# Kernel optimization log

Measured on AMD Instinct MI355X. Metric: run time of the kernel, lower is better.

Reference implementation:

```python
import jax, jax.numpy as jnp
import numpy as np

N = 50000      # nodes
E = 1_600_000  # edges
F_IN = 128; HID = 128; LAT = 64; OUT = 128; GEN = 2


def gcn_conv(x, src, dst, norm, W, b, n_nodes):
    """PyG GCNConv with self-loops already appended to (src, dst) and
    symmetric normalization `norm` precomputed per edge."""
    h = x @ W                                    # [N, out]
    msg = h[src] * norm[:, None]                 # [E+N, out] gather + scale
    out = jax.ops.segment_sum(msg, dst, num_segments=n_nodes)
    return out + b


def _self_loop_norm(edge_index, n_nodes):
    loops = jnp.arange(n_nodes, dtype=edge_index.dtype)
    src = jnp.concatenate([edge_index[0], loops])
    dst = jnp.concatenate([edge_index[1], loops])
    deg = jnp.zeros((n_nodes,), jnp.float32).at[dst].add(1.0)
    dinv = jnp.where(deg > 0, deg ** -0.5, 0.0)
    norm = dinv[src] * dinv[dst]
    return src, dst, norm


def setup_inputs() -> dict:
    key = jax.random.key(0)
    ks = jax.random.split(key, 12)
    p = lambda k, s: jax.random.normal(k, s, jnp.float32) * 0.05
    return {
        "x": jax.random.normal(ks[0], (N, F_IN), jnp.float32),
        "edge_index": jax.random.randint(ks[1], (2, E), 0, N, jnp.int32),
        "eps": jax.random.normal(ks[2], (N, LAT), jnp.float32),
        "u": jax.random.uniform(ks[3], (N, GEN), jnp.float32),
        "W1": p(ks[4], (F_IN, HID)), "b1": jnp.zeros((HID,), jnp.float32),
        "W_mu": p(ks[5], (HID, LAT)), "b_mu": jnp.zeros((LAT,), jnp.float32),
        "W_ls": p(ks[6], (HID, LAT)), "b_ls": jnp.zeros((LAT,), jnp.float32),
        "W_dx": p(ks[7], (LAT, OUT)), "b_dx": jnp.zeros((OUT,), jnp.float32),
        "W_g": p(ks[8], (LAT, GEN)), "b_g": jnp.zeros((GEN,), jnp.float32),
        "W_lc": p(ks[9], (LAT, 1)), "b_lc": jnp.zeros((1,), jnp.float32),
    }


def reference(x, edge_index, eps, u, W1, b1, W_mu, b_mu, W_ls, b_ls,
              W_dx, b_dx, W_g, b_g, W_lc, b_lc):
    n = x.shape[0]
    src, dst, norm = _self_loop_norm(edge_index, n)

    # Encoder: GCN -> relu -> (mu, logvar)
    h = jax.nn.relu(gcn_conv(x, src, dst, norm, W1, b1, n))
    mu = gcn_conv(h, src, dst, norm, W_mu, b_mu, n)
    logvar = gcn_conv(h, src, dst, norm, W_ls, b_ls, n)

    # reparameterize: z = eps * exp(0.5*logvar) + mu
    z = eps * jnp.exp(0.5 * logvar) + mu

    # decoders / classifiers
    recon_x = gcn_conv(z, src, dst, norm, W_dx, b_dx, n)
    logits_gender = gcn_conv(z, src, dst, norm, W_g, b_g, n)
    logits_label = z @ W_lc + b_lc

    # Gumbel-softmax (hard, straight-through), temperature=1.0
    g = -jnp.log(-jnp.log(u + 1e-20) + 1e-20)
    y_soft = jax.nn.softmax(logits_gender + g, axis=-1)
    y_hard = jax.nn.one_hot(jnp.argmax(y_soft, axis=-1), GEN, dtype=y_soft.dtype)
    gender = jax.lax.stop_gradient(y_hard - y_soft) + y_soft

    return (recon_x, gender, logits_label, mu, logvar, z)
```

## Files before the change

### kernel.cpp

```cpp
#include <hip/hip_runtime.h>
#include <hip/hip_fp16.h>
#include <cstddef>


constexpr int R = 200;
constexpr int NBUCK = 250;
constexpr int NBLK = 250;
constexpr int SLABCAP = 12288;

__global__ __launch_bounds__(256, 4) void hist_gemm_kernel(
    const int* __restrict__ dst, int* __restrict__ gh, int e, int chunk,
    const float* __restrict__ A, const float* __restrict__ W,
    __half* __restrict__ Ch, int n) {
  constexpr int K = 128, M = 128, KT = 64, RPT = 4;
  constexpr int CG = M / 4;
  constexpr int RS = 256 / CG;
  constexpr int RPB = RS * RPT;
  __shared__ float sW[KT * M];
  __shared__ int h[NBUCK];

  if (blockIdx.x < (unsigned)NBLK) {
    for (int t = threadIdx.x; t < NBUCK; t += 256) h[t] = 0;
    __syncthreads();
    int beg = blockIdx.x * chunk;
    int fin = min(e, beg + chunk);
    for (int i = beg + threadIdx.x; i < fin; i += 256)
      atomicAdd(&h[dst[i] / R], 1);
    __syncthreads();
    for (int t = threadIdx.x; t < NBUCK; t += 256)
      gh[t * NBLK + blockIdx.x] = h[t];
    return;
  }

  const int bid = blockIdx.x - NBLK;
  const int cg = threadIdx.x % CG;
  const int rs = threadIdx.x / CG;
  const int row0 = bid * RPB + rs * RPT;

  const float* Arow[RPT];
#pragma unroll
  for (int rr = 0; rr < RPT; ++rr) {
    int row = row0 + rr;
    if (row > n - 1) row = n - 1;
    Arow[rr] = A + (size_t)row * K;
  }

  float4 acc[RPT];
#pragma unroll
  for (int rr = 0; rr < RPT; ++rr) acc[rr] = float4{0.f, 0.f, 0.f, 0.f};

  for (int kt = 0; kt < K; kt += KT) {
    if (kt) __syncthreads();
    for (int i = threadIdx.x * 4; i < KT * M; i += 1024)
      *reinterpret_cast<float4*>(&sW[i]) =
          *reinterpret_cast<const float4*>(&W[kt * M + i]);
    __syncthreads();
#pragma unroll 4
    for (int k4 = 0; k4 < KT; k4 += 4) {
      float4 a[RPT];
#pragma unroll
      for (int rr = 0; rr < RPT; ++rr)
        a[rr] = *reinterpret_cast<const float4*>(Arow[rr] + kt + k4);
#pragma unroll
      for (int j = 0; j < 4; ++j) {
        float4 w = *reinterpret_cast<const float4*>(&sW[(k4 + j) * M + cg * 4]);
#pragma unroll
        for (int rr = 0; rr < RPT; ++rr) {
          float av = reinterpret_cast<const float*>(&a[rr])[j];
          acc[rr].x += av * w.x;
          acc[rr].y += av * w.y;
          acc[rr].z += av * w.z;
          acc[rr].w += av * w.w;
        }
      }
    }
  }

#pragma unroll
  for (int rr = 0; rr < RPT; ++rr) {
    int row = row0 + rr;
    if (row < n) {
      __half2* d2 = reinterpret_cast<__half2*>(Ch + (size_t)row * M + cg * 4);
      d2[0] = __floats2half2_rn(acc[rr].x, acc[rr].y);
      d2[1] = __floats2half2_rn(acc[rr].z, acc[rr].w);
    }
  }
}

__global__ __launch_bounds__(256) void bscan_kernel(
    const int* __restrict__ gh, int* __restrict__ ghs,
    int* __restrict__ rowptr_n) {
  __shared__ int s[256];
  __shared__ int sBase[NBUCK + 1];
  const int b = blockIdx.x;
  const int tid = threadIdx.x;

  int tot = 0;
  if (tid < NBUCK) {
    const int* row = gh + tid * NBLK;
    for (int k = 0; k < NBLK; ++k) tot += row[k];
  }
  s[tid] = tot;
  __syncthreads();
  for (int off = 1; off < 256; off <<= 1) {
    int t = (tid >= off) ? s[tid - off] : 0;
    __syncthreads();
    s[tid] += t;
    __syncthreads();
  }
  if (tid < NBUCK) sBase[tid] = s[tid] - tot;
  if (tid == NBUCK - 1) sBase[NBUCK] = s[tid];
  __syncthreads();

  int v = (tid < NBLK) ? gh[b * NBLK + tid] : 0;
  s[tid] = v;
  __syncthreads();
  for (int off = 1; off < 256; off <<= 1) {
    int t = (tid >= off) ? s[tid - off] : 0;
    __syncthreads();
    s[tid] += t;
    __syncthreads();
  }
  if (tid < NBLK) ghs[b * NBLK + tid] = s[tid] - v + sBase[b];
  if (b == 0 && tid == 0) *rowptr_n = sBase[NBUCK];
}

__global__ __launch_bounds__(256) void scatter_kernel(
    const int* __restrict__ src, const int* __restrict__ dst,
    const int* __restrict__ ghs, int* __restrict__ binned, int e, int chunk) {
  __shared__ int cur[NBUCK];
  for (int t = threadIdx.x; t < NBUCK; t += 256)
    cur[t] = ghs[t * NBLK + blockIdx.x];
  __syncthreads();
  int beg = blockIdx.x * chunk;
  int fin = min(e, beg + chunk);
  for (int i = beg + threadIdx.x; i < fin; i += 256) {
    int d = dst[i];
    int b = d / R;
    int p = atomicAdd(&cur[b], 1);
    binned[p] = ((d - b * R) << 16) | src[i];
  }
}

__global__ __launch_bounds__(256) void final_kernel(
    const int* __restrict__ binned, const int* __restrict__ ghs,
    int* __restrict__ rowptr, int* __restrict__ csr,
    float* __restrict__ dinv, int n, int e) {
  __shared__ int sdeg[R];
  __shared__ int sscan[256];
  __shared__ int scur[R];
  __shared__ int slab[SLABCAP];
  const int b = blockIdx.x;
  const int tid = threadIdx.x;
  const int base = ghs[b * NBLK];
  const int end = (b < NBUCK - 1) ? ghs[(b + 1) * NBLK] : e;
  const int cnt = end - base;

  if (tid < R) sdeg[tid] = 0;
  __syncthreads();
  for (int k = base + tid; k < end; k += 256)
    atomicAdd(&sdeg[binned[k] >> 16], 1);
  __syncthreads();

  int dv = (tid < R) ? sdeg[tid] : 0;
  sscan[tid] = dv;
  __syncthreads();
  for (int off = 1; off < 256; off <<= 1) {
    int t = (tid >= off) ? sscan[tid - off] : 0;
    __syncthreads();
    sscan[tid] += t;
    __syncthreads();
  }
  int excl = sscan[tid] - dv;
  int node = b * R + tid;
  if (tid < R && node < n) {
    rowptr[node] = base + excl;
    dinv[node] = 1.0f / sqrtf((float)dv + 1.0f);
    scur[tid] = excl;
  }
  __syncthreads();

  const bool fits = (cnt <= SLABCAP);
  for (int k = base + tid; k < end; k += 256) {
    int rec = binned[k];
    int p = atomicAdd(&scur[rec >> 16], 1);
    int s = rec & 0xFFFF;
    if (fits) slab[p] = s;
    else csr[base + p] = s;
  }
  __syncthreads();
  if (fits)
    for (int k = tid; k < cnt; k += 256) csr[base + k] = slab[k];
}

template <int K, int M, int KT, int RPT, bool BIAS>
__global__ __launch_bounds__(256, 4) void gemm_kernel(
    const float* __restrict__ A, const float* __restrict__ W,
    const float* __restrict__ bias, float* __restrict__ C, int n) {
  constexpr int CG = M / 4;
  constexpr int RS = 256 / CG;
  constexpr int RPB = RS * RPT;
  __shared__ float sW[KT * M];
  const int cg = threadIdx.x % CG;
  const int rs = threadIdx.x / CG;
  const int row0 = blockIdx.x * RPB + rs * RPT;

  const float* Arow[RPT];
#pragma unroll
  for (int rr = 0; rr < RPT; ++rr) {
    int row = row0 + rr;
    if (row > n - 1) row = n - 1;
    Arow[rr] = A + (size_t)row * K;
  }

  float4 acc[RPT];
#pragma unroll
  for (int rr = 0; rr < RPT; ++rr) acc[rr] = float4{0.f, 0.f, 0.f, 0.f};

  for (int kt = 0; kt < K; kt += KT) {
    if (kt) __syncthreads();
    for (int i = threadIdx.x * 4; i < KT * M; i += 1024)
      *reinterpret_cast<float4*>(&sW[i]) =
          *reinterpret_cast<const float4*>(&W[kt * M + i]);
    __syncthreads();
#pragma unroll 4
    for (int k4 = 0; k4 < KT; k4 += 4) {
      float4 a[RPT];
#pragma unroll
      for (int rr = 0; rr < RPT; ++rr)
        a[rr] = *reinterpret_cast<const float4*>(Arow[rr] + kt + k4);
#pragma unroll
      for (int j = 0; j < 4; ++j) {
        float4 w = *reinterpret_cast<const float4*>(&sW[(k4 + j) * M + cg * 4]);
#pragma unroll
        for (int rr = 0; rr < RPT; ++rr) {
          float av = reinterpret_cast<const float*>(&a[rr])[j];
          acc[rr].x += av * w.x;
          acc[rr].y += av * w.y;
          acc[rr].z += av * w.z;
          acc[rr].w += av * w.w;
        }
      }
    }
  }

  float4 bv = float4{0.f, 0.f, 0.f, 0.f};
  if (BIAS) bv = *reinterpret_cast<const float4*>(&bias[cg * 4]);
#pragma unroll
  for (int rr = 0; rr < RPT; ++rr) {
    int row = row0 + rr;
    if (row < n) {
      float4 o = acc[rr];
      if (BIAS) { o.x += bv.x; o.y += bv.y; o.z += bv.z; o.w += bv.w; }
      *reinterpret_cast<float4*>(&C[(size_t)row * M + cg * 4]) = o;
    }
  }
}

template <bool SRCSCALE, bool BIAS, bool RELU, bool HALF_OUT>
__global__ __launch_bounds__(256) void spmm128_kernel(
    const __half* __restrict__ Xs, void* __restrict__ Yout,
    const int* __restrict__ rowptr, const int* __restrict__ csr,
    const float* __restrict__ dinv, const float* __restrict__ bias, int n) {
  int wid = (blockIdx.x * blockDim.x + threadIdx.x) >> 6;
  int lane = threadIdx.x & 63;
  if (wid >= n) return;
  int beg = rowptr[wid];
  int end = rowptr[wid + 1];
  constexpr int U = 8;
  float a0[U], a1[U];
#pragma unroll
  for (int uu = 0; uu < U; ++uu) { a0[uu] = 0.f; a1[uu] = 0.f; }

  for (int base = beg; base < end; base += 64) {
    int m = end - base;
    if (m > 64) m = 64;
    int idx = (lane < m) ? csr[base + lane] : 0;
    int j = 0;
    for (; j + U <= m; j += U) {
      const __half2* rows[U];
      float ds[U];
#pragma unroll
      for (int uu = 0; uu < U; ++uu) {
        int i = __shfl(idx, j + uu, 64);
        rows[uu] = reinterpret_cast<const __half2*>(Xs + (size_t)i * 128);
        if (SRCSCALE) ds[uu] = dinv[i];
      }
      __half2 v[U];
#pragma unroll
      for (int uu = 0; uu < U; ++uu) v[uu] = rows[uu][lane];
#pragma unroll
      for (int uu = 0; uu < U; ++uu) {
        float2 f = __half22float2(v[uu]);
        if (SRCSCALE) {
          a0[uu] += ds[uu] * f.x;
          a1[uu] += ds[uu] * f.y;
        } else {
          a0[uu] += f.x;
          a1[uu] += f.y;
        }
      }
    }
    for (; j < m; ++j) {
      int i = __shfl(idx, j, 64);
      const __half2* row = reinterpret_cast<const __half2*>(Xs + (size_t)i * 128);
      float2 f = __half22float2(row[lane]);
      if (SRCSCALE) {
        float ds = dinv[i];
        a0[0] += ds * f.x;
        a1[0] += ds * f.y;
      } else {
        a0[0] += f.x;
        a1[0] += f.y;
      }
    }
  }

  float t0 = 0.f, t1 = 0.f;
#pragma unroll
  for (int uu = 0; uu < U; ++uu) { t0 += a0[uu]; t1 += a1[uu]; }

  float di = dinv[wid];

  float2 sf = __half22float2(
      reinterpret_cast<const __half2*>(Xs + (size_t)wid * 128)[lane]);
  if (SRCSCALE) {
    t0 += di * sf.x;
    t1 += di * sf.y;
  } else {
    t0 += sf.x;
    t1 += sf.y;
  }

  float r0 = di * t0;
  float r1 = di * t1;
  if (BIAS) { r0 += bias[lane * 2]; r1 += bias[lane * 2 + 1]; }
  if (RELU) { r0 = fmaxf(r0, 0.f); r1 = fmaxf(r1, 0.f); }

  if (HALF_OUT) {
    reinterpret_cast<__half2*>((__half*)Yout + (size_t)wid * 128)[lane] =
        __floats2half2_rn(di * r0, di * r1);
  } else {
    float2 o = {r0, r1};
    reinterpret_cast<float2*>((float*)Yout + (size_t)wid * 128)[lane] = o;
  }
}

__global__ __launch_bounds__(256, 4) void mlz_kernel(
    const float* __restrict__ hagg,
    const float* __restrict__ Wmu, const float* __restrict__ bmu,
    const float* __restrict__ Wls, const float* __restrict__ bls,
    const float* __restrict__ eps, const float* __restrict__ dinv,
    const float* __restrict__ Wg, const float* __restrict__ Wlc,
    const float* __restrict__ blc,
    float* __restrict__ out_mu, float* __restrict__ out_lv,
    float* __restrict__ out_z, unsigned int* __restrict__ zh8,
    float2* __restrict__ zgs, float* __restrict__ out_label, int n) {
  constexpr int K = 128, M = 64, KT = 64, RPT = 4;
  constexpr int CG = M / 4;
  constexpr int RS = 256 / CG;
  constexpr int RPB = RS * RPT;
  __shared__ float sWm[KT * M];
  __shared__ float sWl[KT * M];
  const int cg = threadIdx.x % CG;
  const int rs = threadIdx.x / CG;
  const int row0 = blockIdx.x * RPB + rs * RPT;

  const float* Arow[RPT];
#pragma unroll
  for (int rr = 0; rr < RPT; ++rr) {
    int row = row0 + rr;
    if (row > n - 1) row = n - 1;
    Arow[rr] = hagg + (size_t)row * K;
  }

  float4 am[RPT], al[RPT];
#pragma unroll
  for (int rr = 0; rr < RPT; ++rr) {
    am[rr] = float4{0.f, 0.f, 0.f, 0.f};
    al[rr] = float4{0.f, 0.f, 0.f, 0.f};
  }

  for (int kt = 0; kt < K; kt += KT) {
    if (kt) __syncthreads();
    for (int i = threadIdx.x * 4; i < KT * M; i += 1024) {
      *reinterpret_cast<float4*>(&sWm[i]) =
          *reinterpret_cast<const float4*>(&Wmu[kt * M + i]);
      *reinterpret_cast<float4*>(&sWl[i]) =
          *reinterpret_cast<const float4*>(&Wls[kt * M + i]);
    }
    __syncthreads();
#pragma unroll 2
    for (int k4 = 0; k4 < KT; k4 += 4) {
      float4 a[RPT];
#pragma unroll
      for (int rr = 0; rr < RPT; ++rr)
        a[rr] = *reinterpret_cast<const float4*>(Arow[rr] + kt + k4);
#pragma unroll
      for (int j = 0; j < 4; ++j) {
        float4 wm = *reinterpret_cast<const float4*>(&sWm[(k4 + j) * M + cg * 4]);
        float4 wl = *reinterpret_cast<const float4*>(&sWl[(k4 + j) * M + cg * 4]);
#pragma unroll
        for (int rr = 0; rr < RPT; ++rr) {
          float av = reinterpret_cast<const float*>(&a[rr])[j];
          am[rr].x += av * wm.x; am[rr].y += av * wm.y;
          am[rr].z += av * wm.z; am[rr].w += av * wm.w;
          al[rr].x += av * wl.x; al[rr].y += av * wl.y;
          al[rr].z += av * wl.z; al[rr].w += av * wl.w;
        }
      }
    }
  }

  float4 bm = *reinterpret_cast<const float4*>(&bmu[cg * 4]);
  float4 bl = *reinterpret_cast<const float4*>(&bls[cg * 4]);
  float wg0[4], wg1[4], wlcv[4];
#pragma unroll
  for (int cc = 0; cc < 4; ++cc) {
    int c = cg * 4 + cc;
    wg0[cc] = Wg[c * 2 + 0];
    wg1[cc] = Wg[c * 2 + 1];
    wlcv[cc] = Wlc[c];
  }
  float blc0 = blc[0];

#pragma unroll
  for (int rr = 0; rr < RPT; ++rr) {
    int row = row0 + rr;
    if (row < n) {
      float4 mu4 = {am[rr].x + bm.x, am[rr].y + bm.y,
                    am[rr].z + bm.z, am[rr].w + bm.w};
      float4 lv4 = {al[rr].x + bl.x, al[rr].y + bl.y,
                    al[rr].z + bl.z, al[rr].w + bl.w};
      float4 e4 = *reinterpret_cast<const float4*>(&eps[(size_t)row * 64 + cg * 4]);
      float4 z4 = {e4.x * expf(0.5f * lv4.x) + mu4.x,
                   e4.y * expf(0.5f * lv4.y) + mu4.y,
                   e4.z * expf(0.5f * lv4.z) + mu4.z,
                   e4.w * expf(0.5f * lv4.w) + mu4.w};
      *reinterpret_cast<float4*>(&out_mu[(size_t)row * 64 + cg * 4]) = mu4;
      *reinterpret_cast<float4*>(&out_lv[(size_t)row * 64 + cg * 4]) = lv4;
      *reinterpret_cast<float4*>(&out_z[(size_t)row * 64 + cg * 4]) = z4;
      float di = dinv[row];
      int pw = __builtin_amdgcn_cvt_pk_fp8_f32(di * z4.x, di * z4.y, 0, false);
      pw = __builtin_amdgcn_cvt_pk_fp8_f32(di * z4.z, di * z4.w, pw, true);
      zh8[(size_t)row * 16 + cg] = (unsigned int)pw;
      float pg0 = z4.x * wg0[0] + z4.y * wg0[1] + z4.z * wg0[2] + z4.w * wg0[3];
      float pg1 = z4.x * wg1[0] + z4.y * wg1[1] + z4.z * wg1[2] + z4.w * wg1[3];
      float pl  = z4.x * wlcv[0] + z4.y * wlcv[1] + z4.z * wlcv[2] + z4.w * wlcv[3];
#pragma unroll
      for (int off = 1; off < 16; off <<= 1) {
        pg0 += __shfl_xor(pg0, off, 64);
        pg1 += __shfl_xor(pg1, off, 64);
        pl  += __shfl_xor(pl, off, 64);
      }
      if (cg == 0) {
        zgs[row] = float2{di * pg0, di * pg1};
        out_label[row] = pl + blc0;
      }
    }
  }
}

__device__ __forceinline__ void fp8x4acc(unsigned d, float* a) {
#if defined(__has_builtin) && __has_builtin(__builtin_amdgcn_cvt_pk_f32_fp8)
  typedef float f32x2 __attribute__((ext_vector_type(2)));
  f32x2 lo = __builtin_amdgcn_cvt_pk_f32_fp8((int)d, false);
  f32x2 hi = __builtin_amdgcn_cvt_pk_f32_fp8((int)d, true);
  a[0] += lo.x; a[1] += lo.y; a[2] += hi.x; a[3] += hi.y;
#else
  a[0] += __builtin_amdgcn_cvt_f32_fp8((int)d, 0);
  a[1] += __builtin_amdgcn_cvt_f32_fp8((int)d, 1);
  a[2] += __builtin_amdgcn_cvt_f32_fp8((int)d, 2);
  a[3] += __builtin_amdgcn_cvt_f32_fp8((int)d, 3);
#endif
}

__global__ __launch_bounds__(256) void spmm_zg_kernel(
    const unsigned char* __restrict__ zh8, const float2* __restrict__ zgs,
    float* __restrict__ zagg, const int* __restrict__ rowptr,
    const int* __restrict__ csr, const float* __restrict__ dinv,
    const float* __restrict__ bg, const float* __restrict__ u,
    float* __restrict__ out_gender, int n) {
  int wid = (blockIdx.x * blockDim.x + threadIdx.x) >> 6;
  int lane = threadIdx.x & 63;
  if (wid >= n) return;
  int beg = rowptr[wid];
  int end = rowptr[wid + 1];
  const int g = lane >> 4;
  const int c = lane & 15;
  const int coff = c * 4;

  float accA[4], accB[4];
#pragma unroll
  for (int f = 0; f < 4; ++f) { accA[f] = 0.f; accB[f] = 0.f; }
  float ga0 = 0.f, ga1 = 0.f;

  for (int base = beg; base < end; base += 64) {
    int m = end - base;
    if (m > 64) m = 64;
    int idx = 0;
    if (lane < m) {
      idx = csr[base + lane];
      float2 gz = zgs[idx];
      ga0 += gz.x;
      ga1 += gz.y;
    }
    int j = 0;
    for (; j + 8 <= m; j += 8) {
      int i0 = __shfl(idx, j + g, 64);
      int i1 = __shfl(idx, j + 4 + g, 64);
      unsigned d0 = *reinterpret_cast<const unsigned*>(
          zh8 + (size_t)(unsigned)i0 * 64 + coff);
      unsigned d1 = *reinterpret_cast<const unsigned*>(
          zh8 + (size_t)(unsigned)i1 * 64 + coff);
      fp8x4acc(d0, accA);
      fp8x4acc(d1, accB);
    }
    if (j < m) {
      int e0 = j + g;
      int e1 = j + 4 + g;
      int i0 = __shfl(idx, min(e0, m - 1), 64);
      int i1 = __shfl(idx, min(e1, m - 1), 64);
      unsigned d0 = *reinterpret_cast<const unsigned*>(
          zh8 + (size_t)(unsigned)i0 * 64 + coff);
      unsigned d1 = *reinterpret_cast<const unsigned*>(
          zh8 + (size_t)(unsigned)i1 * 64 + coff);
      if (e0 >= m) d0 = 0u;
      if (e1 >= m) d1 = 0u;
      fp8x4acc(d0, accA);
      fp8x4acc(d1, accB);
    }
  }

  float t[4];
#pragma unroll
  for (int f = 0; f < 4; ++f) t[f] = accA[f] + accB[f];
#pragma unroll
  for (int f = 0; f < 4; ++f) t[f] += __shfl_xor(t[f], 16, 64);
#pragma unroll
  for (int f = 0; f < 4; ++f) t[f] += __shfl_xor(t[f], 32, 64);

  float di = dinv[wid];
  if (lane < 16) {
    unsigned ds = *reinterpret_cast<const unsigned*>(
        zh8 + (size_t)wid * 64 + coff);
    fp8x4acc(ds, t);
    float4 o = {di * t[0], di * t[1], di * t[2], di * t[3]};
    *reinterpret_cast<float4*>(&zagg[(size_t)wid * 64 + 4 * c]) = o;
  }

  for (int off = 32; off > 0; off >>= 1) {
    ga0 += __shfl_xor(ga0, off, 64);
    ga1 += __shfl_xor(ga1, off, 64);
  }
  if (lane == 0) {
    float2 self = zgs[wid];
    ga0 += self.x;
    ga1 += self.y;
    float lg0 = di * ga0 + bg[0];
    float lg1 = di * ga1 + bg[1];
    float u0 = u[(size_t)wid * 2 + 0];
    float u1 = u[(size_t)wid * 2 + 1];
    float g0 = -logf(-logf(u0 + 1e-20f) + 1e-20f);
    float g1 = -logf(-logf(u1 + 1e-20f) + 1e-20f);
    float a0 = lg0 + g0, a1 = lg1 + g1;
    float mx = fmaxf(a0, a1);
    float e0 = expf(a0 - mx), e1 = expf(a1 - mx);
    float s = e0 + e1;
    float y0 = e0 / s, y1 = e1 / s;
    float h0 = (y1 > y0) ? 0.f : 1.f;
    float h1 = 1.f - h0;
    out_gender[(size_t)wid * 2 + 0] = (h0 - y0) + y0;
    out_gender[(size_t)wid * 2 + 1] = (h1 - y1) + y1;
  }
}

extern "C" void kernel_launch(void* const* d_in, const int* in_sizes, int n_in,
                              void* d_out, int out_size, void* d_ws, size_t ws_size,
                              hipStream_t stream) {
  const float* x   = (const float*)d_in[0];
  const int*   ei  = (const int*)d_in[1];
  const float* eps = (const float*)d_in[2];
  const float* u   = (const float*)d_in[3];
  const float* W1  = (const float*)d_in[4];
  const float* b1  = (const float*)d_in[5];
  const float* Wmu = (const float*)d_in[6];
  const float* bmu = (const float*)d_in[7];
  const float* Wls = (const float*)d_in[8];
  const float* bls = (const float*)d_in[9];
  const float* Wdx = (const float*)d_in[10];
  const float* bdx = (const float*)d_in[11];
  const float* Wg  = (const float*)d_in[12];
  const float* bg  = (const float*)d_in[13];
  const float* Wlc = (const float*)d_in[14];
  const float* blc = (const float*)d_in[15];

  const int n = in_sizes[0] / 128;
  const int e = in_sizes[1] / 2;
  const int* esrc = ei;
  const int* edst = ei + e;

  float* out = (float*)d_out;
  float* out_recon  = out;
  float* out_gender = out + (size_t)n * 128;
  float* out_label  = out_gender + (size_t)n * 2;
  float* out_mu     = out_label + n;
  float* out_lv     = out_mu + (size_t)n * 64;
  float* out_z      = out_lv + (size_t)n * 64;

  char* w = (char*)d_ws;
  size_t off = 0;
  auto alloc = [&](size_t bytes) {
    char* p = w + off;
    off = (off + bytes + 255) & ~(size_t)255;
    return p;
  };
  float* dinv  = (float*)alloc((size_t)n * 4);
  int* rowptr  = (int*)alloc((size_t)(n + 1) * 4);
  int* csr     = (int*)alloc((size_t)e * 4);
  int* gh      = (int*)alloc((size_t)NBUCK * NBLK * 4);
  int* ghs     = (int*)alloc((size_t)NBUCK * NBLK * 4);
  __half* Xs   = (__half*)alloc((size_t)n * 128 * 2);
  __half* hb   = (__half*)alloc((size_t)n * 128 * 2);
  float2* zgs  = (float2*)alloc((size_t)n * 8);
  unsigned char* zh8 = (unsigned char*)Xs;
  float* zagg  = (float*)hb;
  float* hagg  = out_recon;
  int* binned  = (int*)out_lv;

  const int chunk = (e + NBLK - 1) / NBLK;
  const int GBLK = (n + 31) / 32;

  hist_gemm_kernel<<<NBLK + GBLK, 256, 0, stream>>>(
      edst, gh, e, chunk, x, W1, Xs, n);
  bscan_kernel<<<NBUCK, 256, 0, stream>>>(gh, ghs, &rowptr[n]);
  scatter_kernel<<<NBLK, 256, 0, stream>>>(esrc, edst, ghs, binned, e, chunk);
  final_kernel<<<NBUCK, 256, 0, stream>>>(binned, ghs, rowptr, csr, dinv, n, e);

  spmm128_kernel<true, true, true, true>
      <<<(n + 3) / 4, 256, 0, stream>>>(Xs, hb, rowptr, csr, dinv, b1, n);
  spmm128_kernel<false, false, false, false>
      <<<(n + 3) / 4, 256, 0, stream>>>(hb, hagg, rowptr, csr, dinv, nullptr, n);
  mlz_kernel<<<(n + 63) / 64, 256, 0, stream>>>(
      hagg, Wmu, bmu, Wls, bls, eps, dinv, Wg, Wlc, blc,
      out_mu, out_lv, out_z, (unsigned int*)zh8, zgs, out_label, n);
  spmm_zg_kernel<<<(n + 3) / 4, 256, 0, stream>>>(
      zh8, (const float2*)zgs, zagg, rowptr, csr, dinv, bg, u, out_gender, n);
  gemm_kernel<64, 128, 64, 4, true>
      <<<GBLK, 256, 0, stream>>>(zagg, Wdx, bdx, out_recon, n);
}
```

Measured before the change: 411.1 us.

## Spread first-layer GEMM tiles across all four CSR-build kernels

The X@W1 GEMM tiles, previously launched only alongside the histogram kernel, are now split across the histogram, bucket-scan, scatter and final CSR-build kernels. Each kernel gets extra blocks that compute a slice of the GEMM, with shared memory overlaid via unions. The aim is to fill idle compute units during the small, latency-bound CSR phases. In exchange, the larger shared-memory footprint and occupancy hints change per-kernel occupancy, and the tile split counts are hand-picked fixed constants.

```diff
diff --git a/kernel.cpp b/kernel.cpp
--- a/kernel.cpp
+++ b/kernel.cpp
@@ -8,34 +8,14 @@
 constexpr int NBLK = 250;
 constexpr int SLABCAP = 12288;
 
-__global__ __launch_bounds__(256, 4) void hist_gemm_kernel(
-    const int* __restrict__ dst, int* __restrict__ gh, int e, int chunk,
-    const float* __restrict__ A, const float* __restrict__ W,
-    __half* __restrict__ Ch, int n) {
-  constexpr int K = 128, M = 128, KT = 64, RPT = 4;
-  constexpr int CG = M / 4;
-  constexpr int RS = 256 / CG;
-  constexpr int RPB = RS * RPT;
-  __shared__ float sW[KT * M];
-  __shared__ int h[NBUCK];
-
-  if (blockIdx.x < (unsigned)NBLK) {
-    for (int t = threadIdx.x; t < NBUCK; t += 256) h[t] = 0;
-    __syncthreads();
-    int beg = blockIdx.x * chunk;
-    int fin = min(e, beg + chunk);
-    for (int i = beg + threadIdx.x; i < fin; i += 256)
-      atomicAdd(&h[dst[i] / R], 1);
-    __syncthreads();
-    for (int t = threadIdx.x; t < NBUCK; t += 256)
-      gh[t * NBLK + blockIdx.x] = h[t];
-    return;
-  }
-
-  const int bid = blockIdx.x - NBLK;
-  const int cg = threadIdx.x % CG;
-  const int rs = threadIdx.x / CG;
-  const int row0 = bid * RPB + rs * RPT;
+__device__ __forceinline__ void gemm_tile32(
+    int tile, const float* __restrict__ A, const float* __restrict__ W,
+    __half* __restrict__ Ch, int n, float* sW) {
+  constexpr int K = 128, M = 128, KT = 64, RPT = 4, CG = 32;
+  const int tid = threadIdx.x;
+  const int cgi = tid % CG;
+  const int rs = tid / CG;
+  const int row0 = tile * 32 + rs * RPT;
 
   const float* Arow[RPT];
 #pragma unroll
@@ -44,14 +24,13 @@
     if (row > n - 1) row = n - 1;
     Arow[rr] = A + (size_t)row * K;
   }
-
   float4 acc[RPT];
 #pragma unroll
   for (int rr = 0; rr < RPT; ++rr) acc[rr] = float4{0.f, 0.f, 0.f, 0.f};
 
   for (int kt = 0; kt < K; kt += KT) {
     if (kt) __syncthreads();
-    for (int i = threadIdx.x * 4; i < KT * M; i += 1024)
+    for (int i = tid * 4; i < KT * M; i += 1024)
       *reinterpret_cast<float4*>(&sW[i]) =
           *reinterpret_cast<const float4*>(&W[kt * M + i]);
     __syncthreads();
@@ -63,134 +42,172 @@
         a[rr] = *reinterpret_cast<const float4*>(Arow[rr] + kt + k4);
 #pragma unroll
       for (int j = 0; j < 4; ++j) {
-        float4 w = *reinterpret_cast<const float4*>(&sW[(k4 + j) * M + cg * 4]);
+        float4 w2 = *reinterpret_cast<const float4*>(&sW[(k4 + j) * M + cgi * 4]);
 #pragma unroll
         for (int rr = 0; rr < RPT; ++rr) {
           float av = reinterpret_cast<const float*>(&a[rr])[j];
-          acc[rr].x += av * w.x;
-          acc[rr].y += av * w.y;
-          acc[rr].z += av * w.z;
-          acc[rr].w += av * w.w;
+          acc[rr].x += av * w2.x; acc[rr].y += av * w2.y;
+          acc[rr].z += av * w2.z; acc[rr].w += av * w2.w;
         }
       }
     }
   }
-
 #pragma unroll
   for (int rr = 0; rr < RPT; ++rr) {
     int row = row0 + rr;
     if (row < n) {
-      __half2* d2 = reinterpret_cast<__half2*>(Ch + (size_t)row * M + cg * 4);
+      __half2* d2 = reinterpret_cast<__half2*>(Ch + (size_t)row * M + cgi * 4);
       d2[0] = __floats2half2_rn(acc[rr].x, acc[rr].y);
       d2[1] = __floats2half2_rn(acc[rr].z, acc[rr].w);
     }
   }
 }
 
-__global__ __launch_bounds__(256) void bscan_kernel(
+union HistSmem { int h[NBUCK]; float sW[64 * 128]; };
+__global__ __launch_bounds__(256, 4) void hist_gemm_kernel(
+    const int* __restrict__ dst, int* __restrict__ gh, int e, int chunk,
+    const float* __restrict__ A, const float* __restrict__ W,
+    __half* __restrict__ Ch, int n, int tbase) {
+  __shared__ HistSmem sm;
+  if (blockIdx.x < (unsigned)NBLK) {
+    for (int t = threadIdx.x; t < NBUCK; t += 256) sm.h[t] = 0;
+    __syncthreads();
+    int beg = blockIdx.x * chunk;
+    int fin = min(e, beg + chunk);
+    for (int i = beg + threadIdx.x; i < fin; i += 256)
+      atomicAdd(&sm.h[dst[i] / R], 1);
+    __syncthreads();
+    for (int t = threadIdx.x; t < NBUCK; t += 256)
+      gh[t * NBLK + blockIdx.x] = sm.h[t];
+  } else {
+    gemm_tile32(tbase + (blockIdx.x - NBLK), A, W, Ch, n, sm.sW);
+  }
+}
+
+union BscanSmem { struct { int s[256]; int sBase[NBUCK + 1]; } b; float sW[64 * 128]; };
+__global__ __launch_bounds__(256, 4) void bscan_gemm_kernel(
     const int* __restrict__ gh, int* __restrict__ ghs,
-    int* __restrict__ rowptr_n) {
-  __shared__ int s[256];
-  __shared__ int sBase[NBUCK + 1];
-  const int b = blockIdx.x;
+    int* __restrict__ rowptr_n,
+    const float* __restrict__ A, const float* __restrict__ W,
+    __half* __restrict__ Ch, int n, int tbase) {
+  __shared__ BscanSmem sm;
   const int tid = threadIdx.x;
-
-  int tot = 0;
-  if (tid < NBUCK) {
-    const int* row = gh + tid * NBLK;
-    for (int k = 0; k < NBLK; ++k) tot += row[k];
-  }
-  s[tid] = tot;
-  __syncthreads();
-  for (int off = 1; off < 256; off <<= 1) {
-    int t = (tid >= off) ? s[tid - off] : 0;
-    __syncthreads();
-    s[tid] += t;
-    __syncthreads();
-  }
-  if (tid < NBUCK) sBase[tid] = s[tid] - tot;
-  if (tid == NBUCK - 1) sBase[NBUCK] = s[tid];
-  __syncthreads();
-
-  int v = (tid < NBLK) ? gh[b * NBLK + tid] : 0;
-  s[tid] = v;
-  __syncthreads();
-  for (int off = 1; off < 256; off <<= 1) {
-    int t = (tid >= off) ? s[tid - off] : 0;
-    __syncthreads();
-    s[tid] += t;
-    __syncthreads();
-  }
-  if (tid < NBLK) ghs[b * NBLK + tid] = s[tid] - v + sBase[b];
-  if (b == 0 && tid == 0) *rowptr_n = sBase[NBUCK];
-}
-
-__global__ __launch_bounds__(256) void scatter_kernel(
+  if (blockIdx.x < (unsigned)NBUCK) {
+    const int b = blockIdx.x;
+    int tot = 0;
+    if (tid < NBUCK) {
+      const int* row = gh + tid * NBLK;
+      for (int k = 0; k < NBLK; ++k) tot += row[k];
+    }
+    sm.b.s[tid] = tot;
+    __syncthreads();
+    for (int off = 1; off < 256; off <<= 1) {
+      int t = (tid >= off) ? sm.b.s[tid - off] : 0;
+      __syncthreads();
+      sm.b.s[tid] += t;
+      __syncthreads();
+    }
+    if (tid < NBUCK) sm.b.sBase[tid] = sm.b.s[tid] - tot;
+    if (tid == NBUCK - 1) sm.b.sBase[NBUCK] = sm.b.s[tid];
+    __syncthreads();
+
+    int v = (tid < NBLK) ? gh[b * NBLK + tid] : 0;
+    sm.b.s[tid] = v;
+    __syncthreads();
+    for (int off = 1; off < 256; off <<= 1) {
+      int t = (tid >= off) ? sm.b.s[tid - off] : 0;
+      __syncthreads();
+      sm.b.s[tid] += t;
+      __syncthreads();
+    }
+    if (tid < NBLK) ghs[b * NBLK + tid] = sm.b.s[tid] - v + sm.b.sBase[b];
+    if (b == 0 && tid == 0) *rowptr_n = sm.b.sBase[NBUCK];
+  } else {
+    gemm_tile32(tbase + (blockIdx.x - NBUCK), A, W, Ch, n, sm.sW);
+  }
+}
+
+union ScatSmem { int cur[NBUCK]; float sW[64 * 128]; };
+__global__ __launch_bounds__(256, 4) void scatter_gemm_kernel(
     const int* __restrict__ src, const int* __restrict__ dst,
-    const int* __restrict__ ghs, int* __restrict__ binned, int e, int chunk) {
-  __shared__ int cur[NBUCK];
-  for (int t = threadIdx.x; t < NBUCK; t += 256)
-    cur[t] = ghs[t * NBLK + blockIdx.x];
-  __syncthreads();
-  int beg = blockIdx.x * chunk;
-  int fin = min(e, beg + chunk);
-  for (int i = beg + threadIdx.x; i < fin; i += 256) {
-    int d = dst[i];
-    int b = d / R;
-    int p = atomicAdd(&cur[b], 1);
-    binned[p] = ((d - b * R) << 16) | src[i];
-  }
-}
-
-__global__ __launch_bounds__(256) void final_kernel(
+    const int* __restrict__ ghs, int* __restrict__ binned, int e, int chunk,
+    const float* __restrict__ A, const float* __restrict__ W,
+    __half* __restrict__ Ch, int n, int tbase) {
+  __shared__ ScatSmem sm;
+  if (blockIdx.x < (unsigned)NBLK) {
+    for (int t = threadIdx.x; t < NBUCK; t += 256)
+      sm.cur[t] = ghs[t * NBLK + blockIdx.x];
+    __syncthreads();
+    int beg = blockIdx.x * chunk;
+    int fin = min(e, beg + chunk);
+    for (int i = beg + threadIdx.x; i < fin; i += 256) {
+      int d = dst[i];
+      int b = d / R;
+      int p = atomicAdd(&sm.cur[b], 1);
+      binned[p] = ((d - b * R) << 16) | src[i];
+    }
+  } else {
+    gemm_tile32(tbase + (blockIdx.x - NBLK), A, W, Ch, n, sm.sW);
+  }
+}
+
+union FinSmem {
+  struct { int sdeg[R]; int sscan[256]; int scur[R]; int slab[SLABCAP]; } f;
+  float sW[64 * 128];
+};
+__global__ __launch_bounds__(256, 3) void final_gemm_kernel(
     const int* __restrict__ binned, const int* __restrict__ ghs,
     int* __restrict__ rowptr, int* __restrict__ csr,
-    float* __restrict__ dinv, int n, int e) {
-  __shared__ int sdeg[R];
-  __shared__ int sscan[256];
-  __shared__ int scur[R];
-  __shared__ int slab[SLABCAP];
-  const int b = blockIdx.x;
+    float* __restrict__ dinv, int n, int e,
+    const float* __restrict__ A, const float* __restrict__ W,
+    __half* __restrict__ Ch, int tbase, int T) {
+  __shared__ FinSmem sm;
   const int tid = threadIdx.x;
-  const int base = ghs[b * NBLK];
-  const int end = (b < NBUCK - 1) ? ghs[(b + 1) * NBLK] : e;
-  const int cnt = end - base;
-
-  if (tid < R) sdeg[tid] = 0;
-  __syncthreads();
-  for (int k = base + tid; k < end; k += 256)
-    atomicAdd(&sdeg[binned[k] >> 16], 1);
-  __syncthreads();
-
-  int dv = (tid < R) ? sdeg[tid] : 0;
-  sscan[tid] = dv;
-  __syncthreads();
-  for (int off = 1; off < 256; off <<= 1) {
-    int t = (tid >= off) ? sscan[tid - off] : 0;
-    __syncthreads();
-    sscan[tid] += t;
-    __syncthreads();
-  }
-  int excl = sscan[tid] - dv;
-  int node = b * R + tid;
-  if (tid < R && node < n) {
-    rowptr[node] = base + excl;
-    dinv[node] = 1.0f / sqrtf((float)dv + 1.0f);
-    scur[tid] = excl;
-  }
-  __syncthreads();
-
-  const bool fits = (cnt <= SLABCAP);
-  for (int k = base + tid; k < end; k += 256) {
-    int rec = binned[k];
-    int p = atomicAdd(&scur[rec >> 16], 1);
-    int s = rec & 0xFFFF;
-    if (fits) slab[p] = s;
-    else csr[base + p] = s;
-  }
-  __syncthreads();
-  if (fits)
-    for (int k = tid; k < cnt; k += 256) csr[base + k] = slab[k];
+  if (blockIdx.x < (unsigned)NBUCK) {
+    const int b = blockIdx.x;
+    const int base = ghs[b * NBLK];
+    const int endv = (b < NBUCK - 1) ? ghs[(b + 1) * NBLK] : e;
+    const int cnt = endv - base;
+
+    if (tid < R) sm.f.sdeg[tid] = 0;
+    __syncthreads();
+    for (int k = base + tid; k < endv; k += 256)
+      atomicAdd(&sm.f.sdeg[binned[k] >> 16], 1);
+    __syncthreads();
+
+    int dv = (tid < R) ? sm.f.sdeg[tid] : 0;
+    sm.f.sscan[tid] = dv;
+    __syncthreads();
+    for (int off = 1; off < 256; off <<= 1) {
+      int t = (tid >= off) ? sm.f.sscan[tid - off] : 0;
+      __syncthreads();
+      sm.f.sscan[tid] += t;
+      __syncthreads();
+    }
+    int excl = sm.f.sscan[tid] - dv;
+    int node = b * R + tid;
+    if (tid < R && node < n) {
+      rowptr[node] = base + excl;
+      dinv[node] = 1.0f / sqrtf((float)dv + 1.0f);
+      sm.f.scur[tid] = excl;
+    }
+    __syncthreads();
+
+    const bool fits = (cnt <= SLABCAP);
+    for (int k = base + tid; k < endv; k += 256) {
+      int rec = binned[k];
+      int p = atomicAdd(&sm.f.scur[rec >> 16], 1);
+      int s = rec & 0xFFFF;
+      if (fits) sm.f.slab[p] = s;
+      else csr[base + p] = s;
+    }
+    __syncthreads();
+    if (fits)
+      for (int k = tid; k < cnt; k += 256) csr[base + k] = sm.f.slab[k];
+  } else {
+    int t0 = tbase + (blockIdx.x - NBUCK);
+    if (t0 < T) gemm_tile32(t0, A, W, Ch, n, sm.sW);
+  }
 }
 
 template <int K, int M, int KT, int RPT, bool BIAS>
@@ -630,12 +647,19 @@
 
   const int chunk = (e + NBLK - 1) / NBLK;
   const int GBLK = (n + 31) / 32;
-
-  hist_gemm_kernel<<<NBLK + GBLK, 256, 0, stream>>>(
-      edst, gh, e, chunk, x, W1, Xs, n);
-  bscan_kernel<<<NBUCK, 256, 0, stream>>>(gh, ghs, &rowptr[n]);
-  scatter_kernel<<<NBLK, 256, 0, stream>>>(esrc, edst, ghs, binned, e, chunk);
-  final_kernel<<<NBUCK, 256, 0, stream>>>(binned, ghs, rowptr, csr, dinv, n, e);
+  const int T = GBLK;
+
+  const int TH = 500, TB = 450, TS = 350;
+  const int TF = T - TH - TB - TS;
+
+  hist_gemm_kernel<<<NBLK + TH, 256, 0, stream>>>(
+      edst, gh, e, chunk, x, W1, Xs, n, 0);
+  bscan_gemm_kernel<<<NBUCK + TB, 256, 0, stream>>>(
+      gh, ghs, &rowptr[n], x, W1, Xs, n, TH);
+  scatter_gemm_kernel<<<NBLK + TS, 256, 0, stream>>>(
+      esrc, edst, ghs, binned, e, chunk, x, W1, Xs, n, TH + TB);
+  final_gemm_kernel<<<NBUCK + TF, 256, 0, stream>>>(
+      binned, ghs, rowptr, csr, dinv, n, e, x, W1, Xs, TH + TB + TS, T);
 
   spmm128_kernel<true, true, true, true>
       <<<(n + 3) / 4, 256, 0, stream>>>(Xs, hb, rowptr, csr, dinv, b1, n);
```

Measured after the change: 397.4 us (median of 3 runs). -3.3%, faster.
